# Optimization experiments

Measured on AMD Instinct MI355X. Metric: run time of the kernel, lower is better.

Reference implementation:

```python
import jax, jax.numpy as jnp
import numpy as np

B, T, D, H = 2, 2048, 1024, 16
Dh = D // H


def _rope(q, k):
    # q, k: (B, H, T, Dh), interleaved even/odd rotation
    t = q.shape[2]
    dh = q.shape[3]
    inv_freq = 1.0 / (10000.0 ** (jnp.arange(0, dh, 2, dtype=jnp.float32) / dh))
    pos = jnp.arange(t, dtype=jnp.float32)
    freqs = pos[:, None] * inv_freq[None, :]          # (T, Dh/2)
    sin = jnp.sin(freqs)[None, None]                  # (1,1,T,Dh/2)
    cos = jnp.cos(freqs)[None, None]

    def rot(x):
        xe, xo = x[..., ::2], x[..., 1::2]
        re = xe * cos - xo * sin
        ro = xe * sin + xo * cos
        return jnp.stack([re, ro], axis=-1).reshape(x.shape)

    return rot(q), rot(k)


def setup_inputs() -> dict:
    key = jax.random.key(0)
    k1, k2, k3 = jax.random.split(key, 3)
    s = 1.0 / np.sqrt(D)
    return {
        "x": jax.random.normal(k1, (B, T, D), dtype=jnp.float32),
        "w_qkv": jax.random.normal(k2, (3 * D, D), dtype=jnp.float32) * s,
        "b_qkv": jnp.zeros((3 * D,), dtype=jnp.float32),
        "w_out": jax.random.normal(k3, (D, D), dtype=jnp.float32) * s,
        "b_out": jnp.zeros((D,), dtype=jnp.float32),
    }


def reference(x, w_qkv, b_qkv, w_out, b_out):
    b, t, d = x.shape
    qkv = x @ w_qkv.T + b_qkv                         # (B,T,3D)
    q, k, v = jnp.split(qkv, 3, axis=-1)
    q = q.reshape(b, t, H, Dh).transpose(0, 2, 1, 3)  # (B,H,T,Dh)
    k = k.reshape(b, t, H, Dh).transpose(0, 2, 1, 3)
    v = v.reshape(b, t, H, Dh).transpose(0, 2, 1, 3)
    q, k = _rope(q, k)
    scores = jnp.einsum("bhtd,bhsd->bhts", q, k) / jnp.sqrt(jnp.float32(Dh))
    causal = jnp.tril(jnp.ones((t, t), dtype=bool))[None, None]
    scores = jnp.where(causal, scores, -jnp.inf)
    probs = jax.nn.softmax(scores, axis=-1)
    out = jnp.einsum("bhts,bhsd->bhtd", probs, v)     # (B,H,T,Dh)
    out = out.transpose(0, 2, 1, 3).reshape(b, t, d)
    return out @ w_out.T + b_out
```

## Files before the change

### kernel.cpp

```cpp
#include <hip/hip_runtime.h>
#include <hip/hip_bf16.h>
#include <math.h>
#include <type_traits>

#define B_ 2
#define T_ 2048
#define D_ 1024
#define H_ 16
#define DH_ 64

typedef __bf16 bf16_t;
typedef bf16_t bf16x8 __attribute__((ext_vector_type(8)));
typedef bf16_t bf16x4 __attribute__((ext_vector_type(4)));
typedef float f32x4 __attribute__((ext_vector_type(4)));

typedef __attribute__((address_space(1))) const void gas_void;
typedef __attribute__((address_space(3))) void las_void;

__device__ __forceinline__ void gld16(const void* g, void* l) {
    __builtin_amdgcn_global_load_lds((gas_void*)g, (las_void*)l, 16, 0, 0);
}

#define WAITALL() asm volatile("s_waitcnt vmcnt(0) lgkmcnt(0)" ::: "memory")
#define BARRIER() do { asm volatile("" ::: "memory"); __builtin_amdgcn_s_barrier(); asm volatile("" ::: "memory"); } while (0)

__global__ __launch_bounds__(256) void cvt3(const float* __restrict__ a,
                                            const float* __restrict__ b,
                                            const float* __restrict__ c,
                                            bf16_t* __restrict__ oa,
                                            bf16_t* __restrict__ ob,
                                            bf16_t* __restrict__ oc,
                                            float2* __restrict__ tab) {
    if (blockIdx.x >= 8192) {
        int j = (blockIdx.x - 8192) * 256 + threadIdx.x;
        int t = j >> 5, d2 = j & 31;
        float invf = exp2f(-(float)d2 * 0.4152410118609203f);
        float ang = (float)t * invf;
        float sn, cs;
        sincosf(ang, &sn, &cs);
        tab[j] = make_float2(cs, sn);
        return;
    }
    int i = blockIdx.x * 256 + threadIdx.x;
    const float* src; bf16_t* dst; int off;
    if (i < 1048576)      { src = a; dst = oa; off = i; }
    else if (i < 1835008) { src = b; dst = ob; off = i - 1048576; }
    else                  { src = c; dst = oc; off = i - 1835008; }
    float4 f = ((const float4*)src)[off];
    bf16x4 v = { (bf16_t)f.x, (bf16_t)f.y, (bf16_t)f.z, (bf16_t)f.w };
    ((bf16x4*)dst)[off] = v;
}

__global__ __launch_bounds__(256, 3) void gemmqkv(const bf16_t* __restrict__ A,
                                                  const bf16_t* __restrict__ Bw,
                                                  const float* __restrict__ bias,
                                                  const float2* __restrict__ tab,
                                                  bf16_t* __restrict__ q_out,
                                                  bf16_t* __restrict__ k_out,
                                                  bf16_t* __restrict__ vt_out) {
    __shared__ __align__(16) char smem[32768];

    int tid = threadIdx.x;
    int lane = tid & 63, wid = tid >> 6;
    int wr = wid >> 1, wc = wid & 1;
    int lr = lane & 15, lk = lane >> 4;

    int l = blockIdx.y * 24 + blockIdx.x;
    int u = (l & 7) * 96 + (l >> 3);
    int bx = u % 24;
    int by = u / 24;

    f32x4 acc[4][4];
    f32x4 z = {0.f, 0.f, 0.f, 0.f};
#pragma unroll
    for (int i = 0; i < 4; i++)
#pragma unroll
        for (int j = 0; j < 4; j++) acc[i][j] = z;

    int cb = (tid & 3) * 16;
    int rT = tid >> 2;
    int sw = cb ^ (((rT >> 1) & 3) << 4);
    const char* gAp  = (const char*)A  + ((size_t)(by * 128 + rT)) * 2048 + sw;
    const char* gAp1 = gAp + (size_t)64 * 2048;
    const char* gBp  = (const char*)Bw + ((size_t)(bx * 128 + rT)) * 2048 + sw;
    const char* gBp1 = gBp + (size_t)64 * 2048;

    auto stg = [&](int par, int kt) __attribute__((always_inline)) {
        char* base = smem + par * 16384;
        gld16(gAp  + kt * 64, base + tid * 16);
        gld16(gAp1 + kt * 64, base + 4096 + tid * 16);
        gld16(gBp  + kt * 64, base + 8192 + tid * 16);
        gld16(gBp1 + kt * 64, base + 12288 + tid * 16);
    };

    int offA[4], offB[4];
#pragma unroll
    for (int m = 0; m < 4; m++) {
        int row = wr * 64 + m * 16 + lr;
        offA[m] = row * 64 + ((lk * 16) ^ (((row >> 1) & 3) << 4));
    }
#pragma unroll
    for (int n = 0; n < 4; n++) {
        int row = wc * 64 + n * 16 + lr;
        offB[n] = 8192 + row * 64 + ((lk * 16) ^ (((row >> 1) & 3) << 4));
    }

    stg(0, 0);
    for (int kt = 0; kt < 32; ++kt) {
        const char* buf = smem + (kt & 1) * 16384;
        WAITALL();
        BARRIER();
        if (kt < 31) stg((kt + 1) & 1, kt + 1);
        bf16x8 Af[4], Bf[4];
#pragma unroll
        for (int m = 0; m < 4; m++) Af[m] = *(const bf16x8*)(buf + offA[m]);
#pragma unroll
        for (int n = 0; n < 4; n++) Bf[n] = *(const bf16x8*)(buf + offB[n]);
        __builtin_amdgcn_s_setprio(1);
#pragma unroll
        for (int m = 0; m < 4; m++)
#pragma unroll
            for (int n = 0; n < 4; n++)
                acc[m][n] = __builtin_amdgcn_mfma_f32_16x16x32_bf16(Af[m], Bf[n], acc[m][n], 0, 0, 0);
        __builtin_amdgcn_s_setprio(0);
    }
    WAITALL();
    BARRIER();

    int m_base = by * 128 + wr * 64;
    int n_base = bx * 128 + wc * 64;
    char* myL = smem + wid * 8192;
    int which = n_base >> 10;
    int h = (n_base & 1023) >> 6;
    int b = m_base >> 11, t0 = m_base & 2047;
    int bh = b * H_ + h;
    if (which == 2) {
#pragma unroll
        for (int m = 0; m < 4; m++)
#pragma unroll
            for (int n = 0; n < 4; n++) {
                int rd = n * 16 + lr;
                float bv = bias[n_base + rd];
#pragma unroll
                for (int j = 0; j < 4; j++) {
                    int ct = m * 16 + lk * 4 + j;
                    int ct2 = (ct & 32) | (((ct >> 2) & 3) << 3) | (((ct >> 4) & 1) << 2) | (ct & 3);
                    int addr = (rd * 128 + ct2 * 2) ^ ((rd & 7) << 4);
                    *(bf16_t*)(myL + addr) = (bf16_t)(acc[m][n][j] + bv);
                }
            }
#pragma unroll
        for (int it = 0; it < 8; it++) {
            int row = it * 8 + (lane >> 3);
            int byt = (lane & 7) * 16;
            bf16x8 val = *(const bf16x8*)(myL + ((row * 128 + byt) ^ ((row & 7) << 4)));
            *(bf16x8*)(vt_out + ((size_t)bh * DH_ + row) * T_ + t0 + (lane & 7) * 8) = val;
        }
    } else {
        bf16_t* dst = which ? k_out : q_out;
        float qscl = which ? 1.0f : 0.18033688011112042f;
#pragma unroll
        for (int m = 0; m < 4; m++)
#pragma unroll
            for (int n = 0; n < 4; n++) {
                int dh = n * 16 + lr;
                float bv = bias[n_base + dh];
                int dh2 = dh >> 1;
                bool even = (dh & 1) == 0;
#pragma unroll
                for (int j = 0; j < 4; j++) {
                    int rt = m * 16 + lk * 4 + j;
                    float v = acc[m][n][j] + bv;
                    float pp = __shfl_xor(v, 1);
                    float2 cs = tab[(t0 + rt) * 32 + dh2];
                    float r = even ? v * cs.x - pp * cs.y : v * cs.x + pp * cs.y;
                    r *= qscl;
                    int addr = (rt * 128 + dh * 2) ^ ((rt & 7) << 4);
                    *(bf16_t*)(myL + addr) = (bf16_t)r;
                }
            }
#pragma unroll
        for (int it = 0; it < 8; it++) {
            int row = it * 8 + (lane >> 3);
            int byt = (lane & 7) * 16;
            bf16x8 val = *(const bf16x8*)(myL + ((row * 128 + byt) ^ ((row & 7) << 4)));
            *(bf16x8*)(dst + ((size_t)bh * T_ + t0 + row) * DH_ + (lane & 7) * 8) = val;
        }
    }
}

__global__ __launch_bounds__(256) void gemm128o(const bf16_t* __restrict__ A,
                                                const bf16_t* __restrict__ Bw,
                                                const float* __restrict__ bias,
                                                float* __restrict__ f_out,
                                                int K, int N) {
    __shared__ __align__(16) char smem[49152];
    char* b0 = smem;
    char* b1 = smem + 16384;
    char* b2 = smem + 32768;

    int tid = threadIdx.x;
    int lane = tid & 63, wid = tid >> 6;
    int wr = wid >> 1, wc = wid & 1;
    int lr = lane & 15, lk = lane >> 4;

    int l = blockIdx.y * gridDim.x + blockIdx.x;
    int chunk = (gridDim.x * gridDim.y) >> 3;
    int u = (l & 7) * chunk + (l >> 3);
    int bx = u % gridDim.x;
    int by = u / gridDim.x;

    f32x4 acc[4][4];
    f32x4 z = {0.f, 0.f, 0.f, 0.f};
#pragma unroll
    for (int i = 0; i < 4; i++)
#pragma unroll
        for (int j = 0; j < 4; j++) acc[i][j] = z;

    const char* Ab = (const char*)(A + (size_t)by * 128 * K);
    const char* Bb = (const char*)(Bw + (size_t)bx * 128 * K);
    const int rowstride = K * 2;

    int p0 = tid * 16;
    int p1 = 4096 + tid * 16;
    int r0 = p0 >> 6, r1 = p1 >> 6;
    int cb0 = (p0 & 63) ^ (((r0 >> 1) & 3) << 4);
    int cb1 = (p1 & 63) ^ (((r1 >> 1) & 3) << 4);
    size_t gA0 = (size_t)r0 * rowstride + cb0;
    size_t gA1 = (size_t)r1 * rowstride + cb1;

    int oa[4], ob[4];
#pragma unroll
    for (int m = 0; m < 4; m++) {
        int row = wr * 64 + m * 16 + lr;
        oa[m] = row * 64 + ((lk * 16) ^ (((row >> 1) & 3) << 4));
    }
#pragma unroll
    for (int n = 0; n < 4; n++) {
        int row = wc * 64 + n * 16 + lr;
        ob[n] = row * 64 + ((lk * 16) ^ (((row >> 1) & 3) << 4));
    }

    auto stg = [&](char* buf, int ks) __attribute__((always_inline)) {
        const char* Ag = Ab + (size_t)ks * 64;
        const char* Bg = Bb + (size_t)ks * 64;
        gld16(Ag + gA0, buf + p0);
        gld16(Ag + gA1, buf + p1);
        gld16(Bg + gA0, buf + 8192 + p0);
        gld16(Bg + gA1, buf + 8192 + p1);
    };

    auto iterf = [&](auto vmc, char* buf, int ks, bool dostage) __attribute__((always_inline)) {
        constexpr int VM = decltype(vmc)::value;
        if constexpr (VM == 8)      asm volatile("s_waitcnt vmcnt(8)" ::: "memory");
        else if constexpr (VM == 4) asm volatile("s_waitcnt vmcnt(4)" ::: "memory");
        else                        asm volatile("s_waitcnt vmcnt(0)" ::: "memory");
        __builtin_amdgcn_s_barrier();
        asm volatile("" ::: "memory");
        bf16x8 Af[4], Bf[4];
#pragma unroll
        for (int m = 0; m < 4; m++) Af[m] = *(const bf16x8*)(buf + oa[m]);
#pragma unroll
        for (int n = 0; n < 4; n++) Bf[n] = *(const bf16x8*)(buf + 8192 + ob[n]);
#pragma unroll
        for (int m = 0; m < 4; m++)
#pragma unroll
            for (int n = 0; n < 4; n++)
                acc[m][n] = __builtin_amdgcn_mfma_f32_16x16x32_bf16(Af[m], Bf[n], acc[m][n], 0, 0, 0);
        asm volatile("" ::: "memory");
        __builtin_amdgcn_s_barrier();
        asm volatile("" ::: "memory");
        if (dostage) stg(buf, ks);
    };

    std::integral_constant<int, 8> c8;
    std::integral_constant<int, 4> c4;
    std::integral_constant<int, 0> c0;

    stg(b0, 0);
    stg(b1, 1);
    stg(b2, 2);
    for (int s = 0; s < 30; s += 3) {
        iterf(c8, b0, s + 3, s + 3 < 32);
        iterf(c8, b1, s + 4, s + 4 < 32);
        iterf(c8, b2, s + 5, s + 5 < 32);
    }
    iterf(c4, b0, 0, false);
    iterf(c0, b1, 0, false);

    int m_base = by * 128 + wr * 64;
    int n_base = bx * 128 + wc * 64;
#pragma unroll
    for (int m = 0; m < 4; m++) {
        int gm0 = m_base + m * 16 + lk * 4;
#pragma unroll
        for (int n = 0; n < 4; n++) {
            int nc = n_base + n * 16 + lr;
            float bv = bias[nc];
#pragma unroll
            for (int j = 0; j < 4; j++)
                f_out[(size_t)(gm0 + j) * N + nc] = acc[m][n][j] + bv;
        }
    }
}

__global__ __launch_bounds__(256, 4) void attn128(const bf16_t* __restrict__ Q,
                                                  const bf16_t* __restrict__ K,
                                                  const bf16_t* __restrict__ Vt,
                                                  bf16_t* __restrict__ Ao) {
    __shared__ __align__(16) char smem[40960];

    int tid = threadIdx.x;
    int lane = tid & 63, wid = tid >> 6;
    int lr = lane & 15, lk = lane >> 4;
    int xcd = blockIdx.x & 7, idx = blockIdx.x >> 3;
    int bh = xcd * 4 + (idx & 3);
    int i4 = idx >> 2;
    int qt = (i4 < 8) ? i4 : 23 - i4;
    int q0 = qt * 128;
    int qrelw = wid * 16 + lr;

    const bf16_t* Qp0 = Q + ((size_t)bh * T_ + q0 + qrelw) * DH_;
    const bf16_t* Qp1 = Qp0 + 64 * DH_;
    bf16x8 qa0 = *(const bf16x8*)(Qp0 + lk * 8);
    bf16x8 qa1 = *(const bf16x8*)(Qp0 + 32 + lk * 8);
    bf16x8 qb0 = *(const bf16x8*)(Qp1 + lk * 8);
    bf16x8 qb1 = *(const bf16x8*)(Qp1 + 32 + lk * 8);

    f32x4 zz = {0.f, 0.f, 0.f, 0.f};
    f32x4 oa0[4], oa1[4];
#pragma unroll
    for (int dt = 0; dt < 4; dt++) { oa0[dt] = zz; oa1[dt] = zz; }
    float ls0 = 0.f, ls1 = 0.f;
    bf16x8 pA0, pA1, pB0, pB1;

    const char* Kbase = (const char*)(K + (size_t)bh * T_ * DH_);
    const char* Vbase = (const char*)(Vt + (size_t)bh * DH_ * T_);

    auto stage = [&](int s, char* Kd, char* Vd) __attribute__((always_inline)) {
        int kv0 = s * 64;
        const char* Kg = Kbase + (size_t)kv0 * 128;
#pragma unroll
        for (int c = 0; c < 2; c++) {
            int o = c * 4096 + tid * 16;
            int r = o >> 7;
            int g = o ^ ((r & 7) << 4);
            gld16(Kg + g, Kd + o);
            gld16(Vbase + (size_t)r * (T_ * 2) + kv0 * 2 + (g & 127), Vd + o);
        }
    };

    auto do_qk = [&](const char* Kc, int m0, int m1) __attribute__((always_inline)) {
#pragma unroll
        for (int kt = 0; kt < 4; kt++) {
            int row = kt * 16 + lr;
            int key = (row & 7) << 4;
            bf16x8 kf0 = *(const bf16x8*)(Kc + ((row * 128 + lk * 16) ^ key));
            bf16x8 kf1 = *(const bf16x8*)(Kc + ((row * 128 + 64 + lk * 16) ^ key));
            if (m0 != 2) {
                f32x4 s = zz;
                s = __builtin_amdgcn_mfma_f32_16x16x32_bf16(kf0, qa0, s, 0, 0, 0);
                s = __builtin_amdgcn_mfma_f32_16x16x32_bf16(kf1, qa1, s, 0, 0, 0);
#pragma unroll
                for (int j = 0; j < 4; j++) {
                    float sv = s[j];
                    if (m0 == 1) {
                        int kv = kt * 16 + lk * 4 + j;
                        sv = (kv <= qrelw) ? sv : -__builtin_inff();
                    }
                    float e = exp2f(sv);
                    ls0 += e;
                    if (kt < 2) pA0[kt * 4 + j] = (bf16_t)e;
                    else        pA1[(kt - 2) * 4 + j] = (bf16_t)e;
                }
            }
            {
                f32x4 s = zz;
                s = __builtin_amdgcn_mfma_f32_16x16x32_bf16(kf0, qb0, s, 0, 0, 0);
                s = __builtin_amdgcn_mfma_f32_16x16x32_bf16(kf1, qb1, s, 0, 0, 0);
#pragma unroll
                for (int j = 0; j < 4; j++) {
                    float sv = s[j];
                    if (m1 == 1) {
                        int kv = kt * 16 + lk * 4 + j;
                        sv = (kv <= qrelw) ? sv : -__builtin_inff();
                    }
                    float e = exp2f(sv);
                    ls1 += e;
                    if (kt < 2) pB0[kt * 4 + j] = (bf16_t)e;
                    else        pB1[(kt - 2) * 4 + j] = (bf16_t)e;
                }
            }
        }
    };

    auto do_pv = [&](const char* Vc, bool g0on) __attribute__((always_inline)) {
#pragma unroll
        for (int dt = 0; dt < 4; dt++) {
            int row = dt * 16 + lr;
            int key = (row & 7) << 4;
            bf16x8 vf0 = *(const bf16x8*)(Vc + ((row * 128 + lk * 16) ^ key));
            bf16x8 vf1 = *(const bf16x8*)(Vc + ((row * 128 + 64 + lk * 16) ^ key));
            if (g0on) {
                f32x4 o = oa0[dt];
                o = __builtin_amdgcn_mfma_f32_16x16x32_bf16(vf0, pA0, o, 0, 0, 0);
                o = __builtin_amdgcn_mfma_f32_16x16x32_bf16(vf1, pA1, o, 0, 0, 0);
                oa0[dt] = o;
            }
            f32x4 o = oa1[dt];
            o = __builtin_amdgcn_mfma_f32_16x16x32_bf16(vf0, pB0, o, 0, 0, 0);
            o = __builtin_amdgcn_mfma_f32_16x16x32_bf16(vf1, pB1, o, 0, 0, 0);
            oa1[dt] = o;
        }
    };

    stage(0, smem, smem + 16384);
    stage(1, smem + 8192, smem + 24576);
    asm volatile("s_waitcnt vmcnt(4)" ::: "memory");
    __builtin_amdgcn_s_barrier();
    asm volatile("" ::: "memory");
    do_qk(smem, qt == 0 ? 1 : 0, 0);

    char* Kr = smem + 8192;
    char* Kw = smem;
    char* Vr = smem + 16384;
    char* Vn = smem + 24576;
    char* Vw = smem + 32768;

    int last = 2 * qt;
    auto iterA = [&](int s, int m0, int m1) __attribute__((always_inline)) {
        WAITALL();
        __builtin_amdgcn_s_barrier();
        asm volatile("" ::: "memory");
        if (s + 2 <= last + 1) stage(s + 2, Kw, Vw);
        do_pv(Vr, true);
        do_qk(Kr, m0, m1);
        char* t;
        t = Kr; Kr = Kw; Kw = t;
        t = Vr; Vr = Vn; Vn = Vw; Vw = t;
    };

    for (int s = 0; s < last - 1; ++s) iterA(s, 0, 0);
    if (qt > 0) iterA(last - 1, 1, 0);
    iterA(last, 2, 1);
    do_pv(Vr, false);
    __syncthreads();

    ls0 += __shfl_xor(ls0, 16); ls0 += __shfl_xor(ls0, 32);
    ls1 += __shfl_xor(ls1, 16); ls1 += __shfl_xor(ls1, 32);
    float ri0 = __builtin_amdgcn_rcpf(ls0);
    float ri1 = __builtin_amdgcn_rcpf(ls1);

    char* myL = smem + wid * 2048;
    int b = bh >> 4, h = bh & 15;
#pragma unroll
    for (int dt = 0; dt < 4; dt++)
#pragma unroll
        for (int j = 0; j < 4; j++) {
            int dh = dt * 16 + lk * 4 + j;
            int addr = (lr * 128 + dh * 2) ^ ((lr & 7) << 4);
            *(bf16_t*)(myL + addr) = (bf16_t)(oa0[dt][j] * ri0);
        }
#pragma unroll
    for (int it = 0; it < 2; it++) {
        int row = it * 8 + (lane >> 3);
        int byt = (lane & 7) * 16;
        bf16x8 val = *(const bf16x8*)(myL + ((row * 128 + byt) ^ ((row & 7) << 4)));
        int t = q0 + wid * 16 + row;
        *(bf16x8*)(Ao + ((size_t)b * T_ + t) * D_ + h * DH_ + (lane & 7) * 8) = val;
    }
#pragma unroll
    for (int dt = 0; dt < 4; dt++)
#pragma unroll
        for (int j = 0; j < 4; j++) {
            int dh = dt * 16 + lk * 4 + j;
            int addr = (lr * 128 + dh * 2) ^ ((lr & 7) << 4);
            *(bf16_t*)(myL + addr) = (bf16_t)(oa1[dt][j] * ri1);
        }
#pragma unroll
    for (int it = 0; it < 2; it++) {
        int row = it * 8 + (lane >> 3);
        int byt = (lane & 7) * 16;
        bf16x8 val = *(const bf16x8*)(myL + ((row * 128 + byt) ^ ((row & 7) << 4)));
        int t = q0 + 64 + wid * 16 + row;
        *(bf16x8*)(Ao + ((size_t)b * T_ + t) * D_ + h * DH_ + (lane & 7) * 8) = val;
    }
}

extern "C" void kernel_launch(void* const* d_in, const int* in_sizes, int n_in,
                              void* d_out, int out_size, void* d_ws, size_t ws_size,
                              hipStream_t stream) {
    const float* x     = (const float*)d_in[0];
    const float* w_qkv = (const float*)d_in[1];
    const float* b_qkv = (const float*)d_in[2];
    const float* w_out = (const float*)d_in[3];
    const float* b_out = (const float*)d_in[4];
    float* out = (float*)d_out;

    char* ws = (char*)d_ws;
    bf16_t* xb    = (bf16_t*)(ws);
    bf16_t* wqkvb = (bf16_t*)(ws + 8388608);
    bf16_t* wob   = (bf16_t*)(ws + 14680064);
    bf16_t* qb    = (bf16_t*)(ws + 16777216);
    bf16_t* kb    = (bf16_t*)(ws + 25165824);
    bf16_t* vtb   = (bf16_t*)(ws + 33554432);
    bf16_t* ab    = (bf16_t*)(ws + 41943040);
    float2* tab   = (float2*)(ws + 41943040);

    cvt3<<<8448, 256, 0, stream>>>(x, w_qkv, w_out, xb, wqkvb, wob, tab);

    gemmqkv<<<dim3(24, 32), 256, 0, stream>>>(xb, wqkvb, b_qkv, tab, qb, kb, vtb);
    attn128<<<512, 256, 0, stream>>>(qb, kb, vtb, ab);
    gemm128o<<<dim3(8, 32), 256, 0, stream>>>(ab, wob, b_out, out, 1024, 1024);
}
```

Before: 111.3 us.

## Triple-buffer QKV GEMM LDS staging with partial vmcnt waits

Replaces the double-buffered K-loop in the QKV projection GEMM with a three-stage LDS ring, prefetching two tiles ahead and waiting only on the oldest loads via partial vmcnt counts. The goal is to hide more global-load latency behind the MFMA work. The change adds a second barrier per iteration, removes the setprio hints and the occupancy hint of 3 blocks per CU, and raises shared memory to 48KB, which may lower occupancy. The vmcnt(8) wait in the last full loop iteration, where nothing new is staged, looks suspicious, though the final vmcnt(0) may still cover it.

```diff
diff --git a/kernel.cpp b/kernel.cpp
--- a/kernel.cpp
+++ b/kernel.cpp
@@ -51,14 +51,17 @@
     ((bf16x4*)dst)[off] = v;
 }
 
-__global__ __launch_bounds__(256, 3) void gemmqkv(const bf16_t* __restrict__ A,
-                                                  const bf16_t* __restrict__ Bw,
-                                                  const float* __restrict__ bias,
-                                                  const float2* __restrict__ tab,
-                                                  bf16_t* __restrict__ q_out,
-                                                  bf16_t* __restrict__ k_out,
-                                                  bf16_t* __restrict__ vt_out) {
-    __shared__ __align__(16) char smem[32768];
+__global__ __launch_bounds__(256) void gemmqkv(const bf16_t* __restrict__ A,
+                                               const bf16_t* __restrict__ Bw,
+                                               const float* __restrict__ bias,
+                                               const float2* __restrict__ tab,
+                                               bf16_t* __restrict__ q_out,
+                                               bf16_t* __restrict__ k_out,
+                                               bf16_t* __restrict__ vt_out) {
+    __shared__ __align__(16) char smem[49152];
+    char* b0 = smem;
+    char* b1 = smem + 16384;
+    char* b2 = smem + 32768;
 
     int tid = threadIdx.x;
     int lane = tid & 63, wid = tid >> 6;
@@ -77,53 +80,76 @@
 #pragma unroll
         for (int j = 0; j < 4; j++) acc[i][j] = z;
 
-    int cb = (tid & 3) * 16;
-    int rT = tid >> 2;
-    int sw = cb ^ (((rT >> 1) & 3) << 4);
-    const char* gAp  = (const char*)A  + ((size_t)(by * 128 + rT)) * 2048 + sw;
-    const char* gAp1 = gAp + (size_t)64 * 2048;
-    const char* gBp  = (const char*)Bw + ((size_t)(bx * 128 + rT)) * 2048 + sw;
-    const char* gBp1 = gBp + (size_t)64 * 2048;
-
-    auto stg = [&](int par, int kt) __attribute__((always_inline)) {
-        char* base = smem + par * 16384;
-        gld16(gAp  + kt * 64, base + tid * 16);
-        gld16(gAp1 + kt * 64, base + 4096 + tid * 16);
-        gld16(gBp  + kt * 64, base + 8192 + tid * 16);
-        gld16(gBp1 + kt * 64, base + 12288 + tid * 16);
-    };
-
-    int offA[4], offB[4];
+    const char* Ab = (const char*)(A + (size_t)by * 128 * 1024);
+    const char* Bb = (const char*)(Bw + (size_t)bx * 128 * 1024);
+    const int rowstride = 2048;
+
+    int p0 = tid * 16;
+    int p1 = 4096 + tid * 16;
+    int r0 = p0 >> 6, r1 = p1 >> 6;
+    int cb0 = (p0 & 63) ^ (((r0 >> 1) & 3) << 4);
+    int cb1 = (p1 & 63) ^ (((r1 >> 1) & 3) << 4);
+    size_t gA0 = (size_t)r0 * rowstride + cb0;
+    size_t gA1 = (size_t)r1 * rowstride + cb1;
+
+    int oa[4], ob[4];
 #pragma unroll
     for (int m = 0; m < 4; m++) {
         int row = wr * 64 + m * 16 + lr;
-        offA[m] = row * 64 + ((lk * 16) ^ (((row >> 1) & 3) << 4));
+        oa[m] = row * 64 + ((lk * 16) ^ (((row >> 1) & 3) << 4));
     }
 #pragma unroll
     for (int n = 0; n < 4; n++) {
         int row = wc * 64 + n * 16 + lr;
-        offB[n] = 8192 + row * 64 + ((lk * 16) ^ (((row >> 1) & 3) << 4));
-    }
-
-    stg(0, 0);
-    for (int kt = 0; kt < 32; ++kt) {
-        const char* buf = smem + (kt & 1) * 16384;
-        WAITALL();
-        BARRIER();
-        if (kt < 31) stg((kt + 1) & 1, kt + 1);
+        ob[n] = 8192 + row * 64 + ((lk * 16) ^ (((row >> 1) & 3) << 4));
+    }
+
+    auto stg = [&](char* buf, int ks) __attribute__((always_inline)) {
+        const char* Ag = Ab + (size_t)ks * 64;
+        const char* Bg = Bb + (size_t)ks * 64;
+        gld16(Ag + gA0, buf + p0);
+        gld16(Ag + gA1, buf + p1);
+        gld16(Bg + gA0, buf + 8192 + p0);
+        gld16(Bg + gA1, buf + 8192 + p1);
+    };
+
+    auto iterf = [&](auto vmc, char* buf, int ks, bool dostage) __attribute__((always_inline)) {
+        constexpr int VM = decltype(vmc)::value;
+        if constexpr (VM == 8)      asm volatile("s_waitcnt vmcnt(8)" ::: "memory");
+        else if constexpr (VM == 4) asm volatile("s_waitcnt vmcnt(4)" ::: "memory");
+        else                        asm volatile("s_waitcnt vmcnt(0)" ::: "memory");
+        __builtin_amdgcn_s_barrier();
+        asm volatile("" ::: "memory");
         bf16x8 Af[4], Bf[4];
 #pragma unroll
-        for (int m = 0; m < 4; m++) Af[m] = *(const bf16x8*)(buf + offA[m]);
-#pragma unroll
-        for (int n = 0; n < 4; n++) Bf[n] = *(const bf16x8*)(buf + offB[n]);
-        __builtin_amdgcn_s_setprio(1);
+        for (int m = 0; m < 4; m++) Af[m] = *(const bf16x8*)(buf + oa[m]);
+#pragma unroll
+        for (int n = 0; n < 4; n++) Bf[n] = *(const bf16x8*)(buf + ob[n]);
 #pragma unroll
         for (int m = 0; m < 4; m++)
 #pragma unroll
             for (int n = 0; n < 4; n++)
                 acc[m][n] = __builtin_amdgcn_mfma_f32_16x16x32_bf16(Af[m], Bf[n], acc[m][n], 0, 0, 0);
-        __builtin_amdgcn_s_setprio(0);
-    }
+        asm volatile("" ::: "memory");
+        __builtin_amdgcn_s_barrier();
+        asm volatile("" ::: "memory");
+        if (dostage) stg(buf, ks);
+    };
+
+    std::integral_constant<int, 8> c8;
+    std::integral_constant<int, 4> c4;
+    std::integral_constant<int, 0> c0;
+
+    stg(b0, 0);
+    stg(b1, 1);
+    stg(b2, 2);
+    for (int s = 0; s < 30; s += 3) {
+        iterf(c8, b0, s + 3, s + 3 < 32);
+        iterf(c8, b1, s + 4, s + 4 < 32);
+        iterf(c8, b2, s + 5, s + 5 < 32);
+    }
+    iterf(c4, b0, 0, false);
+    iterf(c0, b1, 0, false);
     WAITALL();
     BARRIER();
 
```

Result: slower. 114.6 us (+3.0%).
